# Optimization experiments

Hardware: AMD Instinct MI355X
Metric: run time of the kernel (lower is better)

The kernel has to match this reference:

```python
import jax, jax.numpy as jnp
import numpy as np

TOP_K = 2

def setup_inputs() -> dict:
    key = jax.random.key(0)
    ks = jax.random.split(key, 6)
    B, S, D, F, E = 4, 2048, 1024, 4096, 8
    sc = 0.02
    return {
        "x":  jax.random.normal(ks[0], (B, S, D), dtype=jnp.float32),
        "Wg": jax.random.normal(ks[1], (D, E), dtype=jnp.float32) * sc,
        "bg": jnp.zeros((E,), dtype=jnp.float32),
        "W1": jax.random.normal(ks[2], (E, D, F), dtype=jnp.float32) * sc,
        "W3": jax.random.normal(ks[3], (E, D, F), dtype=jnp.float32) * sc,
        "W2": jax.random.normal(ks[4], (E, F, D), dtype=jnp.float32) * sc,
    }

def reference(x, Wg, bg, W1, W3, W2):
    B, S, D = x.shape
    E = Wg.shape[1]
    T = B * S
    # Router: softmax over experts, then top-k of the probabilities (not renormalized)
    logits = jnp.einsum('bsd,de->bse', x, Wg) + bg
    probs = jax.nn.softmax(logits, axis=-1)                 # [B,S,E]
    w, idx = jax.lax.top_k(probs, TOP_K)                    # [B,S,K]
    P_i = probs.mean(axis=(0, 1))                           # [E]

    xf = x.reshape(T, D)
    w_flat = w.reshape(T, TOP_K)
    idx_flat = idx.reshape(T, TOP_K)

    # Aux load-balancing loss
    counts = jnp.zeros((E,), dtype=jnp.float32).at[idx_flat.reshape(-1)].add(1.0)
    f_i = counts / (T * TOP_K)
    aux_loss = E * jnp.dot(f_i, P_i)

    # Dense per-token gate matrix [T,E]: gate is topk prob if expert selected else 0
    gates = jnp.zeros((T, E), dtype=x.dtype)
    gates = gates.at[jnp.arange(T)[:, None], idx_flat].add(w_flat)

    # Per-expert SwiGLU, weighted combine (loop over small fixed E)
    out = jnp.zeros_like(xf)
    for e in range(E):
        h = jax.nn.silu(xf @ W1[e]) * (xf @ W3[e])          # [T,F]
        out = out + (h @ W2[e]) * gates[:, e:e + 1]
    return out.reshape(B, S, D), aux_loss
```

## Files before the change

### kernel.cpp

```cpp
#include <hip/hip_runtime.h>
#include <stdint.h>

#define KT 8192
#define KD 1024
#define KF 4096
#define KE 8

typedef __bf16 bf16x8 __attribute__((ext_vector_type(8)));
typedef float  f32x4  __attribute__((ext_vector_type(4)));

__device__ __forceinline__ unsigned short f2bf(float f) {
  union { float f; uint32_t u; } v; v.f = f;
  uint32_t r = v.u + 0x7fffu + ((v.u >> 16) & 1u);
  return (unsigned short)(r >> 16);
}
__device__ __forceinline__ float bf2f(unsigned short b) {
  union { uint32_t u; float f; } v; v.u = ((uint32_t)b) << 16;
  return v.f;
}
__device__ __forceinline__ void gl_lds16(const void* g, void* l) {
  __builtin_amdgcn_global_load_lds(
      (const __attribute__((address_space(1))) uint32_t*)g,
      (__attribute__((address_space(3))) uint32_t*)l, 16, 0, 0);
}

__global__ __launch_bounds__(256) void k_cvt_x(const float* __restrict__ x,
                                               unsigned short* __restrict__ xb) {
  int i = blockIdx.x * 256 + threadIdx.x;
  float4 v = ((const float4*)x)[i];
  uint2 o;
  o.x = (uint32_t)f2bf(v.x) | ((uint32_t)f2bf(v.y) << 16);
  o.y = (uint32_t)f2bf(v.z) | ((uint32_t)f2bf(v.w) << 16);
  ((uint2*)xb)[i] = o;
}

__global__ __launch_bounds__(256) void k_transpose_cvt(const float* __restrict__ src,
                                                       unsigned short* __restrict__ dst,
                                                       int R, int C) {
  __shared__ unsigned short tile[64][65];
  const int e = blockIdx.z, r0 = blockIdx.y * 64, c0 = blockIdx.x * 64;
  const float* s = src + ((size_t)e * R + r0) * C + c0;
  const int tc = threadIdx.x & 63, tr = threadIdx.x >> 6;
#pragma unroll
  for (int i = 0; i < 16; ++i)
    tile[tr + i * 4][tc] = f2bf(s[(size_t)(tr + i * 4) * C + tc]);
  __syncthreads();
  uint32_t* dp = (uint32_t*)(dst + ((size_t)e * C + c0) * (size_t)R + r0);
  const int dr = threadIdx.x & 31, dc = threadIdx.x >> 5;
  const int Rw = R >> 1;
#pragma unroll
  for (int i = 0; i < 8; ++i) {
    int c = dc + i * 8;
    uint32_t lo = tile[2 * dr][c], hi = tile[2 * dr + 1][c];
    dp[(size_t)c * Rw + dr] = lo | (hi << 16);
  }
}

__global__ __launch_bounds__(256) void k_router(const float* __restrict__ x,
                                                const float* __restrict__ Wg,
                                                const float* __restrict__ bg,
                                                float* __restrict__ Psum,
                                                int* __restrict__ counts,
                                                int* __restrict__ tok_list,
                                                float* __restrict__ gate_list) {
  __shared__ float sWg[KD * 9];
  __shared__ float sbg[8];
  __shared__ float blkP[8];
  const int tid = threadIdx.x;
  for (int i = tid; i < KD * KE; i += 256) sWg[(i >> 3) * 9 + (i & 7)] = Wg[i];
  if (tid < 8) { sbg[tid] = bg[tid]; blkP[tid] = 0.f; }
  __syncthreads();
  const int wave = tid >> 6, lane = tid & 63;
  const int t = blockIdx.x * 4 + wave;
  const float* xr = x + (size_t)t * KD;
  float acc[8];
#pragma unroll
  for (int e2 = 0; e2 < 8; ++e2) acc[e2] = 0.f;
  for (int jj = 0; jj < 16; ++jj) {
    float xv = xr[lane + jj * 64];
    const float* wrow = &sWg[(lane + jj * 64) * 9];
#pragma unroll
    for (int e2 = 0; e2 < 8; ++e2) acc[e2] += xv * wrow[e2];
  }
#pragma unroll
  for (int e2 = 0; e2 < 8; ++e2) {
#pragma unroll
    for (int m = 32; m >= 1; m >>= 1) acc[e2] += __shfl_xor(acc[e2], m, 64);
  }
  if (lane == 0) {
    float lg[8], mx = -1e30f;
#pragma unroll
    for (int e2 = 0; e2 < 8; ++e2) { lg[e2] = acc[e2] + sbg[e2]; mx = fmaxf(mx, lg[e2]); }
    float p[8], ssum = 0.f;
#pragma unroll
    for (int e2 = 0; e2 < 8; ++e2) { p[e2] = __expf(lg[e2] - mx); ssum += p[e2]; }
    float inv = 1.f / ssum;
#pragma unroll
    for (int e2 = 0; e2 < 8; ++e2) { p[e2] *= inv; atomicAdd(&blkP[e2], p[e2]); }
    int i1 = 0;
#pragma unroll
    for (int e2 = 1; e2 < 8; ++e2) if (p[e2] > p[i1]) i1 = e2;
    int i2 = (i1 == 0) ? 1 : 0;
#pragma unroll
    for (int e2 = 0; e2 < 8; ++e2) if (e2 != i1 && p[e2] > p[i2]) i2 = e2;
    int pos1 = atomicAdd(&counts[i1], 1);
    tok_list[i1 * KT + pos1] = t * 2;
    gate_list[i1 * KT + pos1] = p[i1];
    int pos2 = atomicAdd(&counts[i2], 1);
    tok_list[i2 * KT + pos2] = t * 2 + 1;
    gate_list[i2 * KT + pos2] = p[i2];
  }
  __syncthreads();
  if (tid < 8) atomicAdd(&Psum[tid], blkP[tid]);
}

__global__ void k_meta(const int* __restrict__ counts, const float* __restrict__ Psum,
                       int* __restrict__ offsets, int* __restrict__ rb_e,
                       int* __restrict__ rb_r0, int* __restrict__ rb_total,
                       float* __restrict__ aux_out) {
  if (threadIdx.x == 0 && blockIdx.x == 0) {
    int off = 0, nrb = 0;
    for (int e = 0; e < KE; ++e) {
      offsets[e] = off;
      int n = counts[e];
      for (int r0 = 0; r0 < n; r0 += 128) { rb_e[nrb] = e; rb_r0[nrb] = r0; ++nrb; }
      off += n;
    }
    offsets[KE] = off;
    *rb_total = nrb;
    float aux = 0.f;
    for (int e = 0; e < KE; ++e)
      aux += ((float)counts[e] / (float)(KT * 2)) * (Psum[e] / (float)KT);
    aux_out[0] = (float)KE * aux;
  }
}

__global__ __launch_bounds__(256, 2) void k_ffn1(
    const unsigned short* __restrict__ Xbf, const unsigned short* __restrict__ W1t,
    const unsigned short* __restrict__ W3t, const int* __restrict__ tok_list,
    const int* __restrict__ counts, const int* __restrict__ offsets,
    const int* __restrict__ rb_e, const int* __restrict__ rb_r0,
    const int* __restrict__ rb_total, unsigned short* __restrict__ H) {
  const int rb = blockIdx.x;
  if (rb >= *rb_total) return;
  const int n0 = blockIdx.y * 128;
  const int e = rb_e[rb], row0 = rb_r0[rb];
  const int ne = counts[e];
  const int g0 = offsets[e] + row0;

  __shared__ __align__(16) unsigned short sA[128 * 64];
  __shared__ __align__(16) unsigned short sB1[128 * 64];
  __shared__ __align__(16) unsigned short sB3[128 * 64];

  const int tid = threadIdx.x, wave = tid >> 6, lane = tid & 63;
  const int swz = ((lane & 7) ^ (lane >> 3)) * 8;

  size_t aidx[4], bidx[4];
#pragma unroll
  for (int i = 0; i < 4; ++i) {
    int c = wave * 4 + i;
    int r = row0 + c * 8 + (lane >> 3);
    int rr = min(r, ne - 1);
    int tok = tok_list[e * KT + rr] >> 1;
    aidx[i] = (size_t)tok * KD + swz;
    int nrow = c * 8 + (lane >> 3);
    bidx[i] = ((size_t)e * KF + n0 + nrow) * KD + swz;
  }

  const int lm = lane & 15, lk = lane >> 4;
  const int waveM = (wave >> 1) * 64, waveN = (wave & 1) * 64;
  int aoff[2][4], boff[2][4];
#pragma unroll
  for (int ks = 0; ks < 2; ++ks)
#pragma unroll
    for (int t4 = 0; t4 < 4; ++t4) {
      int m = waveM + t4 * 16 + lm;
      aoff[ks][t4] = m * 64 + (((((ks << 2) | lk)) ^ (m & 7)) << 3);
      int n = waveN + t4 * 16 + lm;
      boff[ks][t4] = n * 64 + (((((ks << 2) | lk)) ^ (n & 7)) << 3);
    }

  f32x4 zero = {0.f, 0.f, 0.f, 0.f};
  f32x4 acc1[4][4], acc3[4][4];
#pragma unroll
  for (int a = 0; a < 4; ++a)
#pragma unroll
    for (int b = 0; b < 4; ++b) { acc1[a][b] = zero; acc3[a][b] = zero; }

  for (int k0 = 0; k0 < KD; k0 += 64) {
#pragma unroll
    for (int i = 0; i < 4; ++i) {
      int c = wave * 4 + i;
      gl_lds16(Xbf + aidx[i] + k0, &sA[c * 512 + lane * 8]);
      gl_lds16(W1t + bidx[i] + k0, &sB1[c * 512 + lane * 8]);
      gl_lds16(W3t + bidx[i] + k0, &sB3[c * 512 + lane * 8]);
    }
    __syncthreads();
#pragma unroll
    for (int ks = 0; ks < 2; ++ks) {
      bf16x8 af[4], bf1[4], bf3[4];
#pragma unroll
      for (int t4 = 0; t4 < 4; ++t4) {
        af[t4]  = *(const bf16x8*)&sA[aoff[ks][t4]];
        bf1[t4] = *(const bf16x8*)&sB1[boff[ks][t4]];
        bf3[t4] = *(const bf16x8*)&sB3[boff[ks][t4]];
      }
#pragma unroll
      for (int mt = 0; mt < 4; ++mt)
#pragma unroll
        for (int nt = 0; nt < 4; ++nt) {
          acc1[mt][nt] = __builtin_amdgcn_mfma_f32_16x16x32_bf16(af[mt], bf1[nt], acc1[mt][nt], 0, 0, 0);
          acc3[mt][nt] = __builtin_amdgcn_mfma_f32_16x16x32_bf16(af[mt], bf3[nt], acc3[mt][nt], 0, 0, 0);
        }
    }
    __syncthreads();
  }
#pragma unroll
  for (int mt = 0; mt < 4; ++mt)
#pragma unroll
    for (int reg = 0; reg < 4; ++reg) {
      int r = waveM + mt * 16 + lk * 4 + reg;
      if (row0 + r < ne) {
        size_t base = (size_t)(g0 + r) * KF + n0 + waveN;
#pragma unroll
        for (int nt = 0; nt < 4; ++nt) {
          float h1 = acc1[mt][nt][reg], h3 = acc3[mt][nt][reg];
          float sg = 1.f / (1.f + __expf(-h1));
          H[base + nt * 16 + lm] = f2bf(h1 * sg * h3);
        }
      }
    }
}

__global__ __launch_bounds__(256, 2) void k_ffn2(
    const unsigned short* __restrict__ H, const unsigned short* __restrict__ W2t,
    const int* __restrict__ tok_list, const float* __restrict__ gate_list,
    const int* __restrict__ counts, const int* __restrict__ offsets,
    const int* __restrict__ rb_e, const int* __restrict__ rb_r0,
    const int* __restrict__ rb_total, unsigned short* __restrict__ Obuf) {
  const int rb = blockIdx.x;
  if (rb >= *rb_total) return;
  const int n0 = blockIdx.y * 128;
  const int e = rb_e[rb], row0 = rb_r0[rb];
  const int ne = counts[e];
  const int g0 = offsets[e] + row0;
  const int nrows = ne - row0;

  __shared__ __align__(16) unsigned short sA[128 * 64];
  __shared__ __align__(16) unsigned short sB[128 * 64];

  const int tid = threadIdx.x, wave = tid >> 6, lane = tid & 63;
  const int swz = ((lane & 7) ^ (lane >> 3)) * 8;

  size_t aidx[4], bidx[4];
#pragma unroll
  for (int i = 0; i < 4; ++i) {
    int c = wave * 4 + i;
    int rl = min(c * 8 + (lane >> 3), nrows - 1);
    aidx[i] = (size_t)(g0 + rl) * KF + swz;
    int nrow = c * 8 + (lane >> 3);
    bidx[i] = ((size_t)e * KD + n0 + nrow) * KF + swz;
  }

  const int lm = lane & 15, lk = lane >> 4;
  const int waveM = (wave >> 1) * 64, waveN = (wave & 1) * 64;
  int aoff[2][4], boff[2][4];
#pragma unroll
  for (int ks = 0; ks < 2; ++ks)
#pragma unroll
    for (int t4 = 0; t4 < 4; ++t4) {
      int m = waveM + t4 * 16 + lm;
      aoff[ks][t4] = m * 64 + (((((ks << 2) | lk)) ^ (m & 7)) << 3);
      int n = waveN + t4 * 16 + lm;
      boff[ks][t4] = n * 64 + (((((ks << 2) | lk)) ^ (n & 7)) << 3);
    }

  f32x4 zero = {0.f, 0.f, 0.f, 0.f};
  f32x4 acc[4][4];
#pragma unroll
  for (int a = 0; a < 4; ++a)
#pragma unroll
    for (int b = 0; b < 4; ++b) acc[a][b] = zero;

  for (int k0 = 0; k0 < KF; k0 += 64) {
#pragma unroll
    for (int i = 0; i < 4; ++i) {
      int c = wave * 4 + i;
      gl_lds16(H + aidx[i] + k0, &sA[c * 512 + lane * 8]);
      gl_lds16(W2t + bidx[i] + k0, &sB[c * 512 + lane * 8]);
    }
    __syncthreads();
#pragma unroll
    for (int ks = 0; ks < 2; ++ks) {
      bf16x8 af[4], bf[4];
#pragma unroll
      for (int t4 = 0; t4 < 4; ++t4) {
        af[t4] = *(const bf16x8*)&sA[aoff[ks][t4]];
        bf[t4] = *(const bf16x8*)&sB[boff[ks][t4]];
      }
#pragma unroll
      for (int mt = 0; mt < 4; ++mt)
#pragma unroll
        for (int nt = 0; nt < 4; ++nt)
          acc[mt][nt] = __builtin_amdgcn_mfma_f32_16x16x32_bf16(af[mt], bf[nt], acc[mt][nt], 0, 0, 0);
    }
    __syncthreads();
  }
#pragma unroll
  for (int mt = 0; mt < 4; ++mt)
#pragma unroll
    for (int reg = 0; reg < 4; ++reg) {
      int r = waveM + mt * 16 + lk * 4 + reg;
      if (r < nrows) {
        int li = e * KT + row0 + r;
        float gate = gate_list[li];
        int entry = tok_list[li];
        size_t base = (size_t)entry * KD + n0 + waveN;
#pragma unroll
        for (int nt = 0; nt < 4; ++nt)
          Obuf[base + nt * 16 + lm] = f2bf(acc[mt][nt][reg] * gate);
      }
    }
}

__global__ __launch_bounds__(256) void k_combine(const unsigned short* __restrict__ Obuf,
                                                 float* __restrict__ out) {
  int i = blockIdx.x * 256 + threadIdx.x;
  int t = i >> 8;
  int d = (i & 255) * 4;
  const uint32_t* r0 = (const uint32_t*)(Obuf + ((size_t)t * 2) * KD + d);
  const uint32_t* r1 = (const uint32_t*)(Obuf + ((size_t)t * 2 + 1) * KD + d);
  uint32_t a0 = r0[0], a1 = r0[1], b0 = r1[0], b1 = r1[1];
  float4 o;
  o.x = bf2f(a0 & 0xffff) + bf2f(b0 & 0xffff);
  o.y = bf2f(a0 >> 16)    + bf2f(b0 >> 16);
  o.z = bf2f(a1 & 0xffff) + bf2f(b1 & 0xffff);
  o.w = bf2f(a1 >> 16)    + bf2f(b1 >> 16);
  *(float4*)(out + (size_t)i * 4) = o;
}

extern "C" void kernel_launch(void* const* d_in, const int* in_sizes, int n_in,
                              void* d_out, int out_size, void* d_ws, size_t ws_size,
                              hipStream_t stream) {
  const float* x  = (const float*)d_in[0];
  const float* Wg = (const float*)d_in[1];
  const float* bg = (const float*)d_in[2];
  const float* W1 = (const float*)d_in[3];
  const float* W3 = (const float*)d_in[4];
  const float* W2 = (const float*)d_in[5];
  float* out = (float*)d_out;
  char* ws = (char*)d_ws;

  const size_t OFF_XBF = 0;
  const size_t OFF_W1T = OFF_XBF + (size_t)KT * KD * 2;
  const size_t OFF_W3T = OFF_W1T + (size_t)KE * KD * KF * 2;
  const size_t OFF_W2T = OFF_W3T + (size_t)KE * KD * KF * 2;
  const size_t OFF_H   = OFF_W2T + (size_t)KE * KD * KF * 2;
  const size_t OFF_OB  = OFF_H + (size_t)2 * KT * KF * 2;
  const size_t OFF_CNT = OFF_OB + (size_t)2 * KT * KD * 2;
  const size_t OFF_PS  = OFF_CNT + 32;
  const size_t OFF_OFFS= OFF_CNT + 64;
  const size_t OFF_RBE = OFF_OFFS + 64;
  const size_t OFF_RBR = OFF_RBE + 576;
  const size_t OFF_RBT = OFF_RBR + 576;
  const size_t OFF_TOK = OFF_RBT + 64;
  const size_t OFF_GATE= OFF_TOK + (size_t)KE * KT * 4;
  const size_t WS_NEED = OFF_GATE + (size_t)KE * KT * 4;
  if (ws_size < WS_NEED) return;

  unsigned short* Xbf = (unsigned short*)(ws + OFF_XBF);
  unsigned short* W1t = (unsigned short*)(ws + OFF_W1T);
  unsigned short* W3t = (unsigned short*)(ws + OFF_W3T);
  unsigned short* W2t = (unsigned short*)(ws + OFF_W2T);
  unsigned short* Hb  = (unsigned short*)(ws + OFF_H);
  unsigned short* Ob  = (unsigned short*)(ws + OFF_OB);
  int*   counts   = (int*)(ws + OFF_CNT);
  float* Psum     = (float*)(ws + OFF_PS);
  int*   offsets  = (int*)(ws + OFF_OFFS);
  int*   rb_e     = (int*)(ws + OFF_RBE);
  int*   rb_r0    = (int*)(ws + OFF_RBR);
  int*   rb_total = (int*)(ws + OFF_RBT);
  int*   tok_list = (int*)(ws + OFF_TOK);
  float* gate_list= (float*)(ws + OFF_GATE);

  hipMemsetAsync(ws + OFF_CNT, 0, 64, stream);

  k_cvt_x<<<(KT * KD / 4) / 256, 256, 0, stream>>>(x, Xbf);
  k_transpose_cvt<<<dim3(KF / 64, KD / 64, KE), 256, 0, stream>>>(W1, W1t, KD, KF);
  k_transpose_cvt<<<dim3(KF / 64, KD / 64, KE), 256, 0, stream>>>(W3, W3t, KD, KF);
  k_transpose_cvt<<<dim3(KD / 64, KF / 64, KE), 256, 0, stream>>>(W2, W2t, KF, KD);
  k_router<<<KT / 4, 256, 0, stream>>>(x, Wg, bg, Psum, counts, tok_list, gate_list);
  k_meta<<<1, 64, 0, stream>>>(counts, Psum, offsets, rb_e, rb_r0, rb_total,
                               out + (size_t)KT * KD);
  k_ffn1<<<dim3(136, KF / 128), 256, 0, stream>>>(Xbf, W1t, W3t, tok_list, counts,
                                                  offsets, rb_e, rb_r0, rb_total, Hb);
  k_ffn2<<<dim3(136, KD / 128), 256, 0, stream>>>(Hb, W2t, tok_list, gate_list, counts,
                                                  offsets, rb_e, rb_r0, rb_total, Ob);
  k_combine<<<(KT * KD / 4) / 256, 256, 0, stream>>>(Ob, out);
}
```

Measured before the change: 1.201 ms.

## Fuse x bf16 conversion into router, remap workgroups, widen FFN2 tile to 256

The separate x-to-bf16 conversion kernel is removed, and the router now writes the bf16 copy of x while it reads x for the gating dot products. FFN1 and FFN2 remap their linear workgroup id with an interleave of stride 8, likely meant to spread neighbouring blocks across XCDs for better L2 locality. FFN2 now uses a 128x256 output tile, so each wave holds 4x8 accumulators. This halves the number of blocks and the re-reads of H, at the cost of more registers and LDS per block and fewer blocks in flight.

```diff
diff --git a/kernel.cpp b/kernel.cpp
--- a/kernel.cpp
+++ b/kernel.cpp
@@ -22,16 +22,6 @@
   __builtin_amdgcn_global_load_lds(
       (const __attribute__((address_space(1))) uint32_t*)g,
       (__attribute__((address_space(3))) uint32_t*)l, 16, 0, 0);
-}
-
-__global__ __launch_bounds__(256) void k_cvt_x(const float* __restrict__ x,
-                                               unsigned short* __restrict__ xb) {
-  int i = blockIdx.x * 256 + threadIdx.x;
-  float4 v = ((const float4*)x)[i];
-  uint2 o;
-  o.x = (uint32_t)f2bf(v.x) | ((uint32_t)f2bf(v.y) << 16);
-  o.y = (uint32_t)f2bf(v.z) | ((uint32_t)f2bf(v.w) << 16);
-  ((uint2*)xb)[i] = o;
 }
 
 __global__ __launch_bounds__(256) void k_transpose_cvt(const float* __restrict__ src,
@@ -59,6 +49,7 @@
 __global__ __launch_bounds__(256) void k_router(const float* __restrict__ x,
                                                 const float* __restrict__ Wg,
                                                 const float* __restrict__ bg,
+                                                unsigned short* __restrict__ xb,
                                                 float* __restrict__ Psum,
                                                 int* __restrict__ counts,
                                                 int* __restrict__ tok_list,
@@ -78,6 +69,7 @@
   for (int e2 = 0; e2 < 8; ++e2) acc[e2] = 0.f;
   for (int jj = 0; jj < 16; ++jj) {
     float xv = xr[lane + jj * 64];
+    xb[(size_t)t * KD + lane + jj * 64] = f2bf(xv);
     const float* wrow = &sWg[(lane + jj * 64) * 9];
 #pragma unroll
     for (int e2 = 0; e2 < 8; ++e2) acc[e2] += xv * wrow[e2];
@@ -141,9 +133,13 @@
     const int* __restrict__ counts, const int* __restrict__ offsets,
     const int* __restrict__ rb_e, const int* __restrict__ rb_r0,
     const int* __restrict__ rb_total, unsigned short* __restrict__ H) {
-  const int rb = blockIdx.x;
+  const int gx = gridDim.x;
+  const int nwg = gx * gridDim.y;
+  int lid = blockIdx.x + gx * blockIdx.y;
+  lid = (lid & 7) * (nwg >> 3) + (lid >> 3);
+  const int rb = lid % gx;
   if (rb >= *rb_total) return;
-  const int n0 = blockIdx.y * 128;
+  const int n0 = (lid / gx) * 128;
   const int e = rb_e[rb], row0 = rb_r0[rb];
   const int ne = counts[e];
   const int g0 = offsets[e] + row0;
@@ -238,71 +234,72 @@
     const int* __restrict__ counts, const int* __restrict__ offsets,
     const int* __restrict__ rb_e, const int* __restrict__ rb_r0,
     const int* __restrict__ rb_total, unsigned short* __restrict__ Obuf) {
-  const int rb = blockIdx.x;
+  const int gx = gridDim.x;
+  const int nwg = gx * gridDim.y;
+  int lid = blockIdx.x + gx * blockIdx.y;
+  lid = (lid & 7) * (nwg >> 3) + (lid >> 3);
+  const int rb = lid % gx;
   if (rb >= *rb_total) return;
-  const int n0 = blockIdx.y * 128;
+  const int n0 = (lid / gx) * 256;
   const int e = rb_e[rb], row0 = rb_r0[rb];
   const int ne = counts[e];
   const int g0 = offsets[e] + row0;
   const int nrows = ne - row0;
 
   __shared__ __align__(16) unsigned short sA[128 * 64];
-  __shared__ __align__(16) unsigned short sB[128 * 64];
+  __shared__ __align__(16) unsigned short sB[256 * 64];
 
   const int tid = threadIdx.x, wave = tid >> 6, lane = tid & 63;
   const int swz = ((lane & 7) ^ (lane >> 3)) * 8;
 
-  size_t aidx[4], bidx[4];
+  const unsigned short* Wb = W2t + (size_t)e * KD * KF;
+  uint32_t aoff[4], boff[8];
 #pragma unroll
   for (int i = 0; i < 4; ++i) {
     int c = wave * 4 + i;
     int rl = min(c * 8 + (lane >> 3), nrows - 1);
-    aidx[i] = (size_t)(g0 + rl) * KF + swz;
+    aoff[i] = (uint32_t)(g0 + rl) * KF + swz;
+  }
+#pragma unroll
+  for (int i = 0; i < 8; ++i) {
+    int c = wave * 8 + i;
     int nrow = c * 8 + (lane >> 3);
-    bidx[i] = ((size_t)e * KD + n0 + nrow) * KF + swz;
+    boff[i] = (uint32_t)(n0 + nrow) * KF + swz;
   }
 
   const int lm = lane & 15, lk = lane >> 4;
-  const int waveM = (wave >> 1) * 64, waveN = (wave & 1) * 64;
-  int aoff[2][4], boff[2][4];
-#pragma unroll
-  for (int ks = 0; ks < 2; ++ks)
-#pragma unroll
-    for (int t4 = 0; t4 < 4; ++t4) {
-      int m = waveM + t4 * 16 + lm;
-      aoff[ks][t4] = m * 64 + (((((ks << 2) | lk)) ^ (m & 7)) << 3);
-      int n = waveN + t4 * 16 + lm;
-      boff[ks][t4] = n * 64 + (((((ks << 2) | lk)) ^ (n & 7)) << 3);
-    }
+  const int waveM = (wave >> 1) * 64, waveN = (wave & 1) * 128;
 
   f32x4 zero = {0.f, 0.f, 0.f, 0.f};
-  f32x4 acc[4][4];
+  f32x4 acc[4][8];
 #pragma unroll
   for (int a = 0; a < 4; ++a)
 #pragma unroll
-    for (int b = 0; b < 4; ++b) acc[a][b] = zero;
+    for (int b = 0; b < 8; ++b) acc[a][b] = zero;
 
   for (int k0 = 0; k0 < KF; k0 += 64) {
 #pragma unroll
-    for (int i = 0; i < 4; ++i) {
-      int c = wave * 4 + i;
-      gl_lds16(H + aidx[i] + k0, &sA[c * 512 + lane * 8]);
-      gl_lds16(W2t + bidx[i] + k0, &sB[c * 512 + lane * 8]);
-    }
+    for (int i = 0; i < 4; ++i)
+      gl_lds16(H + aoff[i] + k0, &sA[(wave * 4 + i) * 512 + lane * 8]);
+#pragma unroll
+    for (int i = 0; i < 8; ++i)
+      gl_lds16(Wb + boff[i] + k0, &sB[(wave * 8 + i) * 512 + lane * 8]);
     __syncthreads();
 #pragma unroll
     for (int ks = 0; ks < 2; ++ks) {
-      bf16x8 af[4], bf[4];
-#pragma unroll
-      for (int t4 = 0; t4 < 4; ++t4) {
-        af[t4] = *(const bf16x8*)&sA[aoff[ks][t4]];
-        bf[t4] = *(const bf16x8*)&sB[boff[ks][t4]];
-      }
+      const int ko = ((((ks << 2) | lk) ^ (lm & 7)) << 3);
+      bf16x8 af[4], bfr[8];
+#pragma unroll
+      for (int t = 0; t < 4; ++t)
+        af[t] = *(const bf16x8*)&sA[(waveM + t * 16 + lm) * 64 + ko];
+#pragma unroll
+      for (int t = 0; t < 8; ++t)
+        bfr[t] = *(const bf16x8*)&sB[(waveN + t * 16 + lm) * 64 + ko];
 #pragma unroll
       for (int mt = 0; mt < 4; ++mt)
 #pragma unroll
-        for (int nt = 0; nt < 4; ++nt)
-          acc[mt][nt] = __builtin_amdgcn_mfma_f32_16x16x32_bf16(af[mt], bf[nt], acc[mt][nt], 0, 0, 0);
+        for (int nt = 0; nt < 8; ++nt)
+          acc[mt][nt] = __builtin_amdgcn_mfma_f32_16x16x32_bf16(af[mt], bfr[nt], acc[mt][nt], 0, 0, 0);
     }
     __syncthreads();
   }
@@ -317,7 +314,7 @@
         int entry = tok_list[li];
         size_t base = (size_t)entry * KD + n0 + waveN;
 #pragma unroll
-        for (int nt = 0; nt < 4; ++nt)
+        for (int nt = 0; nt < 8; ++nt)
           Obuf[base + nt * 16 + lm] = f2bf(acc[mt][nt][reg] * gate);
       }
     }
@@ -385,16 +382,15 @@
 
   hipMemsetAsync(ws + OFF_CNT, 0, 64, stream);
 
-  k_cvt_x<<<(KT * KD / 4) / 256, 256, 0, stream>>>(x, Xbf);
   k_transpose_cvt<<<dim3(KF / 64, KD / 64, KE), 256, 0, stream>>>(W1, W1t, KD, KF);
   k_transpose_cvt<<<dim3(KF / 64, KD / 64, KE), 256, 0, stream>>>(W3, W3t, KD, KF);
   k_transpose_cvt<<<dim3(KD / 64, KF / 64, KE), 256, 0, stream>>>(W2, W2t, KF, KD);
-  k_router<<<KT / 4, 256, 0, stream>>>(x, Wg, bg, Psum, counts, tok_list, gate_list);
+  k_router<<<KT / 4, 256, 0, stream>>>(x, Wg, bg, Xbf, Psum, counts, tok_list, gate_list);
   k_meta<<<1, 64, 0, stream>>>(counts, Psum, offsets, rb_e, rb_r0, rb_total,
                                out + (size_t)KT * KD);
   k_ffn1<<<dim3(136, KF / 128), 256, 0, stream>>>(Xbf, W1t, W3t, tok_list, counts,
                                                   offsets, rb_e, rb_r0, rb_total, Hb);
-  k_ffn2<<<dim3(136, KD / 128), 256, 0, stream>>>(Hb, W2t, tok_list, gate_list, counts,
+  k_ffn2<<<dim3(136, KD / 256), 256, 0, stream>>>(Hb, W2t, tok_list, gate_list, counts,
                                                   offsets, rb_e, rb_r0, rb_total, Ob);
   k_combine<<<(KT * KD / 4) / 256, 256, 0, stream>>>(Ob, out);
 }
```

New measurement: 1.203 ms. Within noise of the previous version (+0.1%).
